# Kernel optimization log

Hardware: AMD Instinct MI355X
Metric: run time of the kernel (lower is better)

Reference implementation:

```python
import jax, jax.numpy as jnp
import numpy as np

B, L, N = 32, 64, 8
C, H_IMG, W_IMG = 3, 40, 40
HID = 64
N_ACT = 8
CNN_OUT = 64  # 64 channels * 1 * 1 spatial after the three convs on 40x40


def _conv(x, w, b, stride):
    # x: (B', Cin, H, W), w: (Cout, Cin, kh, kw)
    y = jax.lax.conv_general_dilated(
        x, w, window_strides=(stride, stride), padding='VALID',
        dimension_numbers=('NCHW', 'OIHW', 'NCHW'))
    return y + b[None, :, None, None]


def setup_inputs() -> dict:
    key = jax.random.key(0)
    ks = jax.random.split(key, 12)

    def rn(k, shape, fan_in):
        return jax.random.normal(k, shape, dtype=jnp.float32) * (1.0 / np.sqrt(fan_in))

    inp = {
        'obs_batch': jax.random.normal(ks[0], (B, L, N, C, H_IMG, W_IMG), dtype=jnp.float32),
        'hidden_state': jnp.zeros((B, N, HID), dtype=jnp.float32),
        'conv1_w': rn(ks[1], (32, C, 8, 8), C * 8 * 8),
        'conv1_b': jnp.zeros((32,), jnp.float32),
        'conv2_w': rn(ks[2], (64, 32, 4, 4), 32 * 4 * 4),
        'conv2_b': jnp.zeros((64,), jnp.float32),
        'conv3_w': rn(ks[3], (64, 64, 3, 3), 64 * 3 * 3),
        'conv3_b': jnp.zeros((64,), jnp.float32),
        'w_ih': rn(ks[4], (3 * HID, CNN_OUT), CNN_OUT),
        'w_hh': rn(ks[5], (3 * HID, HID), HID),
        'b_ih': jnp.zeros((3 * HID,), jnp.float32),
        'b_hh': jnp.zeros((3 * HID,), jnp.float32),
        'fc_w': rn(ks[6], (N_ACT, HID), HID),
        'fc_b': jnp.zeros((N_ACT,), jnp.float32),
    }
    return inp


def reference(obs_batch, hidden_state, conv1_w, conv1_b, conv2_w, conv2_b,
              conv3_w, conv3_b, w_ih, w_hh, b_ih, b_hh, fc_w, fc_b):
    b, l, n = obs_batch.shape[:3]
    x = obs_batch.reshape(-1, C, H_IMG, W_IMG)            # (B*L*N, C, H, W)
    x = jax.nn.relu(_conv(x, conv1_w, conv1_b, 4))
    x = jax.nn.relu(_conv(x, conv2_w, conv2_b, 2))
    x = jax.nn.relu(_conv(x, conv3_w, conv3_b, 1))
    feats = x.reshape(b, l, n, -1)                        # (B, L, N, F)

    # (L, B*N, F) time-major for scan
    rnn_in = feats.transpose(1, 0, 2, 3).reshape(l, b * n, -1)
    h0 = hidden_state.reshape(b * n, HID)

    def step(h, xt):
        gi = xt @ w_ih.T + b_ih
        gh = h @ w_hh.T + b_hh
        i_r, i_z, i_n = jnp.split(gi, 3, axis=-1)
        h_r, h_z, h_n = jnp.split(gh, 3, axis=-1)
        r = jax.nn.sigmoid(i_r + h_r)
        z = jax.nn.sigmoid(i_z + h_z)
        nn_ = jnp.tanh(i_n + r * h_n)
        h_new = (1.0 - z) * nn_ + z * h
        return h_new, h_new

    h_last, hs = jax.lax.scan(step, h0, rnn_in)           # hs: (L, B*N, HID)

    # torch path: stack (L, B*N, H) -> permute to (B*N, L, H) -> reshape (B*L*N, H)
    rnn_out = hs.transpose(1, 0, 2).reshape(b, n, l, HID).transpose(0, 2, 1, 3)
    q = rnn_out.reshape(-1, HID) @ fc_w.T + fc_b
    q_values = q.reshape(b, l, n, N_ACT)
    next_hidden_state = h_last.reshape(b, n, HID)
    return q_values, next_hidden_state
```

## Files before the change

### kernel.cpp

```cpp
#include <hip/hip_runtime.h>
#include <math.h>

typedef unsigned short ushort_t;
typedef unsigned int uint_t;
typedef __attribute__((ext_vector_type(8))) short short8_t;
typedef __attribute__((ext_vector_type(4))) float f32x4_t;

constexpr int Bb = 32, Ll = 64, Nn = 8;
constexpr int IMGS = Bb * Ll * Nn;
constexpr int Cc = 3, Hh = 40, Ww = 40;
constexpr int HID = 64, G3 = 192, NACT = 8;

__device__ inline float bf2f(ushort_t u) {
  union { uint_t i; float f; } v; v.i = ((uint_t)u) << 16; return v.f;
}
__device__ inline ushort_t f2bf(float f) {
  union { float f; uint_t u; } v; v.f = f;
  uint_t r = v.u + 0x7fffu + ((v.u >> 16) & 1u);
  return (ushort_t)(r >> 16);
}
__device__ inline void unpack2(uint_t u, float& lo, float& hi) {
  union { uint_t i; float f; } a, b;
  a.i = u << 16; b.i = u & 0xffff0000u;
  lo = a.f; hi = b.f;
}
__device__ inline float ld1(const void* p, int idx, int isbf) {
  return isbf ? bf2f(((const ushort_t*)p)[idx]) : ((const float*)p)[idx];
}
__device__ inline short8_t ldsh8(const ushort_t* p) {
  union { short8_t v; uint2 u[2]; } r;
  r.u[0] = *(const uint2*)p;
  r.u[1] = *(const uint2*)(p + 4);
  return r.v;
}
__device__ inline short8_t ldg8(const ushort_t* p) {
  union { short8_t v; uint4 u; } r;
  r.u = *(const uint4*)p;
  return r.v;
}
#define WAVE_FENCE() asm volatile("s_waitcnt lgkmcnt(0)" ::: "memory")

__global__ __launch_bounds__(256) void detect_kernel(
    const ushort_t* __restrict__ obs, const ushort_t* __restrict__ whh,
    int* __restrict__ flags) {
  __shared__ int cnt[2];
  if (threadIdx.x < 2) cnt[threadIdx.x] = 0;
  __syncthreads();
  int bad0 = 0, bad1 = 0;
  for (int i = threadIdx.x; i < 4096; i += 256) {
    int e0 = (obs[i] >> 7) & 0xFF; if (e0 >= 0xC0) bad0++;
    int e1 = (whh[i] >> 7) & 0xFF; if (e1 >= 0xC0) bad1++;
  }
  atomicAdd(&cnt[0], bad0);
  atomicAdd(&cnt[1], bad1);
  __syncthreads();
  if (threadIdx.x == 0) { flags[0] = (cnt[0] <= 4); flags[1] = (cnt[1] <= 4); }
}

__global__ __launch_bounds__(256) void repack_kernel(
    const void* __restrict__ w1, const void* __restrict__ w2,
    const void* __restrict__ w3, const void* __restrict__ wih,
    const int* __restrict__ flags,
    ushort_t* __restrict__ w1pack, ushort_t* __restrict__ w2pack,
    ushort_t* __restrict__ w3bf, ushort_t* __restrict__ wihb) {
  const int fw = flags[1];
  int t = blockIdx.x * 256 + threadIdx.x;
  if (t < 6144) w1pack[t] = f2bf(ld1(w1, t, fw));
  if (t < 32768) {
    int oc = t >> 9, r = t & 511;
    int kykx = r >> 5, ic = r & 31;
    w2pack[t] = f2bf(ld1(w2, oc * 512 + ic * 16 + kykx, fw));
  }
  if (t < 36864) w3bf[t] = f2bf(ld1(w3, t, fw));
  if (t < 12288) wihb[t] = f2bf(ld1(wih, t, fw));
}

__global__ __launch_bounds__(256, 4) void conv12_kernel(
    const void* __restrict__ obs, const ushort_t* __restrict__ w1pack,
    const ushort_t* __restrict__ w2pack,
    const void* __restrict__ b1, const void* __restrict__ b2,
    const int* __restrict__ flags, ushort_t* __restrict__ f2g, int img_base) {
  __shared__ __attribute__((aligned(16))) ushort_t s_mem[4][4800];

  const int tid = threadIdx.x;
  const int wave = tid >> 6, lane = tid & 63;
  const int lrow = lane & 15, lk8 = lane >> 4;
  const int fobs = flags[0], fw = flags[1];
  const int img0 = blockIdx.x * 4;

  if (fobs) {
    const uint4* src = reinterpret_cast<const uint4*>((const ushort_t*)obs + ((size_t)img_base + img0) * 4800);
    uint4 r[10];
#pragma unroll
    for (int it = 0; it < 10; ++it) {
      const int i = it * 256 + tid;
      r[it] = src[i < 2400 ? i : 2399];
    }
#pragma unroll
    for (int it = 0; it < 10; ++it) {
      const int i = it * 256 + tid;
      if (i < 2400) {
        const int im_ = i / 600, e = i - im_ * 600;
        reinterpret_cast<uint4*>(s_mem[im_])[e] = r[it];
      }
    }
  } else {
    const float4* src = reinterpret_cast<const float4*>((const float*)obs + ((size_t)img_base + img0) * 4800);
#pragma unroll
    for (int bb = 0; bb < 2; ++bb) {
      float4 r[10];
#pragma unroll
      for (int it = 0; it < 10; ++it) {
        const int i = (bb * 10 + it) * 256 + tid;
        r[it] = src[i < 4800 ? i : 4799];
      }
#pragma unroll
      for (int it = 0; it < 10; ++it) {
        const int i = (bb * 10 + it) * 256 + tid;
        if (i < 4800) {
          const int im_ = i / 1200, e = i - im_ * 1200;
          uint2 o;
          o.x = (uint_t)f2bf(r[it].x) | ((uint_t)f2bf(r[it].y) << 16);
          o.y = (uint_t)f2bf(r[it].z) | ((uint_t)f2bf(r[it].w) << 16);
          reinterpret_cast<uint2*>(s_mem[im_])[e] = o;
        }
      }
    }
  }
  __syncthreads();

  {
    ushort_t* si = s_mem[wave];
    int ab[6];
#pragma unroll
    for (int mt = 0; mt < 6; ++mt) {
      int p = mt * 16 + lrow; if (p > 80) p = 80;
      ab[mt] = (p / 9) * 160 + (p % 9) * 4;
    }
    f32x4_t acc[2][6];
#pragma unroll
    for (int nt = 0; nt < 2; ++nt)
#pragma unroll
      for (int mt = 0; mt < 6; ++mt) acc[nt][mt] = (f32x4_t){0.f, 0.f, 0.f, 0.f};
    const ushort_t* wr0 = w1pack + lrow * 192 + lk8 * 8;
#pragma unroll
    for (int ks = 0; ks < 6; ++ks) {
      const int g = ks * 4 + lk8;
      const int aoff = (g >> 3) * 1600 + (g & 7) * 40;
      short8_t b0 = ldg8(wr0 + ks * 32);
      short8_t b1v = ldg8(wr0 + 16 * 192 + ks * 32);
#pragma unroll
      for (int mt = 0; mt < 6; ++mt) {
        short8_t a = ldsh8(&si[aoff + ab[mt]]);
        acc[0][mt] = __builtin_amdgcn_mfma_f32_16x16x32_bf16(a, b0, acc[0][mt], 0, 0, 0);
        acc[1][mt] = __builtin_amdgcn_mfma_f32_16x16x32_bf16(a, b1v, acc[1][mt], 0, 0, 0);
      }
    }
    WAVE_FENCE();
    const float bz0 = ld1(b1, lrow, fw), bz1 = ld1(b1, 16 + lrow, fw);
#pragma unroll
    for (int mt = 0; mt < 6; ++mt) {
#pragma unroll
      for (int r = 0; r < 4; ++r) {
        const int p = mt * 16 + lk8 * 4 + r;
        if (p < 81) {
          si[p * 40 + lrow]      = f2bf(fmaxf(acc[0][mt][r] + bz0, 0.f));
          si[p * 40 + 16 + lrow] = f2bf(fmaxf(acc[1][mt][r] + bz1, 0.f));
        }
      }
    }
  }
  __syncthreads();

  {
    int imgr[3], pbx[3];
#pragma unroll
    for (int mt = 0; mt < 3; ++mt) {
      int row = mt * 16 + lrow; if (row > 35) row = 35;
      const int ir = row / 9, p2 = row - ir * 9;
      imgr[mt] = ir;
      pbx[mt] = (p2 / 3) * 18 + (p2 % 3) * 2;
    }
    f32x4_t acc[3];
#pragma unroll
    for (int mt = 0; mt < 3; ++mt) acc[mt] = (f32x4_t){0.f, 0.f, 0.f, 0.f};
    const ushort_t* w2r = w2pack + (wave * 16 + lrow) * 512 + lk8 * 8;
#pragma unroll
    for (int s = 0; s < 16; ++s) {
      const int po = (s >> 2) * 9 + (s & 3);
      short8_t bv = ldg8(w2r + s * 32);
      short8_t a0 = ldsh8(&s_mem[imgr[0]][(pbx[0] + po) * 40 + lk8 * 8]);
      short8_t a1 = ldsh8(&s_mem[imgr[1]][(pbx[1] + po) * 40 + lk8 * 8]);
      short8_t a2 = ldsh8(&s_mem[imgr[2]][(pbx[2] + po) * 40 + lk8 * 8]);
      acc[0] = __builtin_amdgcn_mfma_f32_16x16x32_bf16(a0, bv, acc[0], 0, 0, 0);
      acc[1] = __builtin_amdgcn_mfma_f32_16x16x32_bf16(a1, bv, acc[1], 0, 0, 0);
      acc[2] = __builtin_amdgcn_mfma_f32_16x16x32_bf16(a2, bv, acc[2], 0, 0, 0);
    }
    const int oc = wave * 16 + lrow;
    const float bias = ld1(b2, oc, fw);
#pragma unroll
    for (int mt = 0; mt < 3; ++mt) {
#pragma unroll
      for (int r = 0; r < 4; ++r) {
        const int row = mt * 16 + lk8 * 4 + r;
        if (row < 36) {
          const int ir = row / 9, pp = row - ir * 9;
          s_mem[ir][3232 + oc * 9 + pp] = f2bf(fmaxf(acc[mt][r] + bias, 0.f));
        }
      }
    }
  }
  __syncthreads();

#pragma unroll
  for (int t2 = 0; t2 < 2; ++t2) {
    const int i = t2 * 256 + tid;
    if (i < 288) {
      const int im_ = i / 72, off = i - im_ * 72;
      *reinterpret_cast<uint4*>(&f2g[((size_t)img_base + img0 + im_) * 576 + off * 8]) =
          *reinterpret_cast<const uint4*>(&s_mem[im_][3232 + off * 8]);
    }
  }
}

__global__ __launch_bounds__(256) void conv3gi_kernel(
    const ushort_t* __restrict__ f2g, const ushort_t* __restrict__ w3bf,
    const ushort_t* __restrict__ wihb, const void* __restrict__ b3,
    const int* __restrict__ flags, float* __restrict__ gi, int img_base) {
  __shared__ __attribute__((aligned(16))) ushort_t f2b[16 * 592];
  __shared__ __attribute__((aligned(16))) ushort_t f3b[16 * 72];

  const int tid = threadIdx.x;
  const int wave = tid >> 6, lane = tid & 63;
  const int lrow = lane & 15, lk8 = lane >> 4;
  const int fw = flags[1];
  const int iloc0 = blockIdx.x * 16;

  for (int i = tid; i < 16 * 72; i += 256) {
    const int im_ = i / 72, off = i - im_ * 72;
    *reinterpret_cast<uint4*>(&f2b[im_ * 592 + off * 8]) =
        *reinterpret_cast<const uint4*>(&f2g[((size_t)img_base + iloc0 + im_) * 576 + off * 8]);
  }
  __syncthreads();

  {
    f32x4_t c3 = (f32x4_t){0.f, 0.f, 0.f, 0.f};
    const ushort_t* w3r = w3bf + (wave * 16 + lrow) * 576 + lk8 * 8;
#pragma unroll
    for (int ks = 0; ks < 18; ++ks) {
      short8_t a = ldsh8(&f2b[lrow * 592 + ks * 32 + lk8 * 8]);
      short8_t bv = ldg8(w3r + ks * 32);
      c3 = __builtin_amdgcn_mfma_f32_16x16x32_bf16(a, bv, c3, 0, 0, 0);
    }
    const int oc = wave * 16 + lrow;
    const float bias = ld1(b3, oc, fw);
#pragma unroll
    for (int r = 0; r < 4; ++r)
      f3b[(lk8 * 4 + r) * 72 + oc] = f2bf(fmaxf(c3[r] + bias, 0.f));
  }
  __syncthreads();

#pragma unroll
  for (int t = 0; t < 3; ++t) {
    const int nt = wave * 3 + t;
    f32x4_t g = (f32x4_t){0.f, 0.f, 0.f, 0.f};
#pragma unroll
    for (int ks = 0; ks < 2; ++ks) {
      short8_t a = ldsh8(&f3b[lrow * 72 + ks * 32 + lk8 * 8]);
      short8_t bv = ldg8(wihb + (nt * 16 + lrow) * 64 + ks * 32 + lk8 * 8);
      g = __builtin_amdgcn_mfma_f32_16x16x32_bf16(a, bv, g, 0, 0, 0);
    }
#pragma unroll
    for (int r = 0; r < 4; ++r)
      gi[((size_t)img_base + iloc0 + lk8 * 4 + r) * G3 + nt * 16 + lrow] = g[r];
  }
}

__global__ __launch_bounds__(64, 1) void gru_kernel(
    const float* __restrict__ gi, const void* __restrict__ h0,
    const void* __restrict__ whh, const void* __restrict__ bih,
    const void* __restrict__ bhh, const int* __restrict__ flags,
    float* __restrict__ rnn, float* __restrict__ hout) {
  __shared__ float s_h[HID];
  const int j = threadIdx.x;
  const int s = blockIdx.x;
  const int fw = flags[1];

  float4 wr[16], wz[16], wn[16];
  if (fw) {
    const uint4* wb = reinterpret_cast<const uint4*>(whh);
#pragma unroll
    for (int i = 0; i < 8; ++i) {
      uint4 a = wb[(size_t)j * 8 + i];
      unpack2(a.x, wr[2 * i].x, wr[2 * i].y);
      unpack2(a.y, wr[2 * i].z, wr[2 * i].w);
      unpack2(a.z, wr[2 * i + 1].x, wr[2 * i + 1].y);
      unpack2(a.w, wr[2 * i + 1].z, wr[2 * i + 1].w);
      uint4 b = wb[(size_t)(64 + j) * 8 + i];
      unpack2(b.x, wz[2 * i].x, wz[2 * i].y);
      unpack2(b.y, wz[2 * i].z, wz[2 * i].w);
      unpack2(b.z, wz[2 * i + 1].x, wz[2 * i + 1].y);
      unpack2(b.w, wz[2 * i + 1].z, wz[2 * i + 1].w);
      uint4 c = wb[(size_t)(128 + j) * 8 + i];
      unpack2(c.x, wn[2 * i].x, wn[2 * i].y);
      unpack2(c.y, wn[2 * i].z, wn[2 * i].w);
      unpack2(c.z, wn[2 * i + 1].x, wn[2 * i + 1].y);
      unpack2(c.w, wn[2 * i + 1].z, wn[2 * i + 1].w);
    }
  } else {
    const float4* wf = reinterpret_cast<const float4*>(whh);
#pragma unroll
    for (int i = 0; i < 16; ++i) {
      wr[i] = wf[(size_t)j * 16 + i];
      wz[i] = wf[(size_t)(64 + j) * 16 + i];
      wn[i] = wf[(size_t)(128 + j) * 16 + i];
    }
  }

  float h = ld1(h0, s * HID + j, fw);
  s_h[j] = h;
  const float bir = ld1(bih, j, fw), biz = ld1(bih, 64 + j, fw), bin_ = ld1(bih, 128 + j, fw);
  const float bhr = ld1(bhh, j, fw), bhz = ld1(bhh, 64 + j, fw), bhn = ld1(bhh, 128 + j, fw);
  const int b = s >> 3, n = s & 7;
  const float* gbase = gi + ((size_t)b * Ll * Nn + n) * G3;
  float* rbase = rnn + ((size_t)b * Ll * Nn + n) * HID;
  WAVE_FENCE();

  float g0 = gbase[j], g1 = gbase[64 + j], g2 = gbase[128 + j];

  for (int l = 0; l < Ll; ++l) {
    float p0 = 0.f, p1 = 0.f, p2 = 0.f;
    if (l + 1 < Ll) {
      const float* gn = gbase + (size_t)(l + 1) * Nn * G3;
      p0 = gn[j]; p1 = gn[64 + j]; p2 = gn[128 + j];
    }
    float hr = bhr, hz = bhz, hn = bhn;
#pragma unroll
    for (int k = 0; k < 16; ++k) {
      float4 hv = *reinterpret_cast<const float4*>(&s_h[k * 4]);
      hr += wr[k].x * hv.x + wr[k].y * hv.y + wr[k].z * hv.z + wr[k].w * hv.w;
      hz += wz[k].x * hv.x + wz[k].y * hv.y + wz[k].z * hv.z + wz[k].w * hv.w;
      hn += wn[k].x * hv.x + wn[k].y * hv.y + wn[k].z * hv.z + wn[k].w * hv.w;
    }
    const float gr = g0 + bir + hr;
    const float gz = g1 + biz + hz;
    const float gn_ = g2 + bin_;
    const float r = 1.f / (1.f + __expf(-gr));
    const float z = 1.f / (1.f + __expf(-gz));
    const float nn_ = tanhf(gn_ + r * hn);
    h = (1.f - z) * nn_ + z * h;
    WAVE_FENCE();
    s_h[j] = h;
    rbase[(size_t)l * Nn * HID + j] = h;
    WAVE_FENCE();
    g0 = p0; g1 = p1; g2 = p2;
  }
  hout[(size_t)s * HID + j] = h;
}

__global__ __launch_bounds__(64) void fc_kernel(
    const float* __restrict__ rnn, const void* __restrict__ fcw,
    const void* __restrict__ fcb, const int* __restrict__ flags,
    float* __restrict__ q) {
  __shared__ float s_w[NACT * HID];
  __shared__ float s_b[NACT];
  const int tid = threadIdx.x;
  const int fw = flags[1];
  for (int i = tid; i < NACT * HID; i += 64) s_w[i] = ld1(fcw, i, fw);
  if (tid < NACT) s_b[tid] = ld1(fcb, tid, fw);
  __syncthreads();
  const int row = blockIdx.x * 64 + tid;
  float x[64];
  const float4* xp = reinterpret_cast<const float4*>(rnn + (size_t)row * HID);
#pragma unroll
  for (int i = 0; i < 16; ++i) {
    float4 v = xp[i];
    x[4 * i] = v.x; x[4 * i + 1] = v.y; x[4 * i + 2] = v.z; x[4 * i + 3] = v.w;
  }
#pragma unroll
  for (int a = 0; a < NACT; ++a) {
    float v = s_b[a];
#pragma unroll
    for (int k = 0; k < 64; ++k) v += x[k] * s_w[a * 64 + k];
    q[(size_t)row * NACT + a] = v;
  }
}

extern "C" void kernel_launch(void* const* d_in, const int* in_sizes, int n_in,
                              void* d_out, int out_size, void* d_ws, size_t ws_size,
                              hipStream_t stream) {
  const void* obs = d_in[0];
  const void* h0  = d_in[1];
  const void* w1  = d_in[2];
  const void* b1  = d_in[3];
  const void* w2  = d_in[4];
  const void* b2  = d_in[5];
  const void* w3  = d_in[6];
  const void* b3  = d_in[7];
  const void* wih = d_in[8];
  const void* whh = d_in[9];
  const void* bih = d_in[10];
  const void* bhh = d_in[11];
  const void* fcw = d_in[12];
  const void* fcb = d_in[13];

  float* qout = (float*)d_out;
  float* hout = qout + (size_t)IMGS * NACT;

  char* wsb = (char*)d_ws;
  int*      flags  = (int*)wsb;
  float*    gi     = (float*)(wsb + 16);
  float*    rnn    = gi + (size_t)IMGS * G3;
  ushort_t* w1pack = (ushort_t*)(rnn + (size_t)IMGS * HID);
  ushort_t* w2pack = w1pack + 6144;
  ushort_t* w3bf   = w2pack + 32768;
  ushort_t* wihb   = w3bf + 36864;
  ushort_t* f2g    = wihb + 12288;

  detect_kernel<<<1, 256, 0, stream>>>((const ushort_t*)obs, (const ushort_t*)whh, flags);
  repack_kernel<<<144, 256, 0, stream>>>(w1, w2, w3, wih, flags, w1pack, w2pack, w3bf, wihb);

  conv12_kernel<<<IMGS / 4, 256, 0, stream>>>(obs, w1pack, w2pack, b1, b2, flags, f2g, 0);
  conv3gi_kernel<<<IMGS / 16, 256, 0, stream>>>(f2g, w3bf, wihb, b3, flags, gi, 0);

  gru_kernel<<<256, 64, 0, stream>>>(gi, h0, whh, bih, bhh, flags, rnn, hout);
  fc_kernel<<<IMGS / 64, 64, 0, stream>>>(rnn, fcw, fcb, flags, qout);
}
```

Measured before the change: 197.0 us.

## Make conv12 persistent with double-buffered prefetch of next image pair

Converts conv12 from one block per 4 images to a persistent grid of 1024 blocks, each looping over image pairs with two LDS buffers. Global loads for the next pair are issued into registers before the current pair's conv1/conv2 MFMA work and written to the alternate buffer afterwards, hiding input-load latency. Work per block shrinks to 2 images, with waves splitting conv1 tiles, which costs extra barriers per iteration and more registers held for prefetch (the launch bounds still request 4 blocks per SM).

```diff
diff --git a/kernel.cpp b/kernel.cpp
--- a/kernel.cpp
+++ b/kernel.cpp
@@ -10,6 +10,8 @@
 constexpr int IMGS = Bb * Ll * Nn;
 constexpr int Cc = 3, Hh = 40, Ww = 40;
 constexpr int HID = 64, G3 = 192, NACT = 8;
+constexpr int CGRID = 1024;
+constexpr int NITER = (IMGS / 2) / CGRID;
 
 __device__ inline float bf2f(ushort_t u) {
   union { uint_t i; float f; } v; v.i = ((uint_t)u) << 16; return v.f;
@@ -79,147 +81,169 @@
     const void* __restrict__ obs, const ushort_t* __restrict__ w1pack,
     const ushort_t* __restrict__ w2pack,
     const void* __restrict__ b1, const void* __restrict__ b2,
-    const int* __restrict__ flags, ushort_t* __restrict__ f2g, int img_base) {
-  __shared__ __attribute__((aligned(16))) ushort_t s_mem[4][4800];
+    const int* __restrict__ flags, ushort_t* __restrict__ f2g) {
+  __shared__ __attribute__((aligned(16))) ushort_t s_mem[2][2][4800];
 
   const int tid = threadIdx.x;
   const int wave = tid >> 6, lane = tid & 63;
   const int lrow = lane & 15, lk8 = lane >> 4;
+  const int im = wave >> 1, half = wave & 1;
   const int fobs = flags[0], fw = flags[1];
-  const int img0 = blockIdx.x * 4;
-
-  if (fobs) {
-    const uint4* src = reinterpret_cast<const uint4*>((const ushort_t*)obs + ((size_t)img_base + img0) * 4800);
-    uint4 r[10];
-#pragma unroll
-    for (int it = 0; it < 10; ++it) {
-      const int i = it * 256 + tid;
-      r[it] = src[i < 2400 ? i : 2399];
-    }
-#pragma unroll
-    for (int it = 0; it < 10; ++it) {
-      const int i = it * 256 + tid;
-      if (i < 2400) {
-        const int im_ = i / 600, e = i - im_ * 600;
-        reinterpret_cast<uint4*>(s_mem[im_])[e] = r[it];
-      }
-    }
-  } else {
-    const float4* src = reinterpret_cast<const float4*>((const float*)obs + ((size_t)img_base + img0) * 4800);
-#pragma unroll
-    for (int bb = 0; bb < 2; ++bb) {
-      float4 r[10];
-#pragma unroll
-      for (int it = 0; it < 10; ++it) {
-        const int i = (bb * 10 + it) * 256 + tid;
-        r[it] = src[i < 4800 ? i : 4799];
-      }
-#pragma unroll
-      for (int it = 0; it < 10; ++it) {
-        const int i = (bb * 10 + it) * 256 + tid;
-        if (i < 4800) {
-          const int im_ = i / 1200, e = i - im_ * 1200;
+
+  int ab[3];
+#pragma unroll
+  for (int t = 0; t < 3; ++t) {
+    int p = (half * 3 + t) * 16 + lrow; if (p > 80) p = 80;
+    ab[t] = (p / 9) * 160 + (p % 9) * 4;
+  }
+  const float bz0 = ld1(b1, lrow, fw), bz1 = ld1(b1, 16 + lrow, fw);
+  int imgr[2], pbx[2];
+#pragma unroll
+  for (int mt = 0; mt < 2; ++mt) {
+    int row = mt * 16 + lrow; if (row > 17) row = 17;
+    const int ir = row / 9, p2 = row - ir * 9;
+    imgr[mt] = ir;
+    pbx[mt] = (p2 / 3) * 18 + (p2 % 3) * 2;
+  }
+  const ushort_t* w1r = w1pack + lrow * 192 + lk8 * 8;
+  const ushort_t* w2r = w2pack + (wave * 16 + lrow) * 512 + lk8 * 8;
+  const float b2v = ld1(b2, wave * 16 + lrow, fw);
+
+  {
+    const size_t base = (size_t)blockIdx.x * 2 * 4800;
+    if (fobs) {
+      const uint4* src = reinterpret_cast<const uint4*>((const ushort_t*)obs + base);
+#pragma unroll
+      for (int t2 = 0; t2 < 5; ++t2) {
+        const int i = t2 * 256 + tid;
+        if (i < 1200) reinterpret_cast<uint4*>(&s_mem[0][i / 600][0])[i % 600] = src[i];
+      }
+    } else {
+      const float4* src = reinterpret_cast<const float4*>((const float*)obs + base);
+#pragma unroll
+      for (int t2 = 0; t2 < 10; ++t2) {
+        const int i = t2 * 256 + tid;
+        if (i < 2400) {
+          float4 v = src[i];
           uint2 o;
-          o.x = (uint_t)f2bf(r[it].x) | ((uint_t)f2bf(r[it].y) << 16);
-          o.y = (uint_t)f2bf(r[it].z) | ((uint_t)f2bf(r[it].w) << 16);
-          reinterpret_cast<uint2*>(s_mem[im_])[e] = o;
+          o.x = (uint_t)f2bf(v.x) | ((uint_t)f2bf(v.y) << 16);
+          o.y = (uint_t)f2bf(v.z) | ((uint_t)f2bf(v.w) << 16);
+          reinterpret_cast<uint2*>(&s_mem[0][i / 1200][0])[i % 1200] = o;
         }
       }
     }
   }
   __syncthreads();
 
-  {
-    ushort_t* si = s_mem[wave];
-    int ab[6];
-#pragma unroll
-    for (int mt = 0; mt < 6; ++mt) {
-      int p = mt * 16 + lrow; if (p > 80) p = 80;
-      ab[mt] = (p / 9) * 160 + (p % 9) * 4;
-    }
-    f32x4_t acc[2][6];
+  for (int it = 0; it < NITER; ++it) {
+    const int c = it & 1;
+    const int img0 = (blockIdx.x + it * CGRID) * 2;
+    const bool has_next = (it + 1 < NITER);
+    const size_t nbase = has_next ? (size_t)(blockIdx.x + (it + 1) * CGRID) * 2 * 4800 : 0;
+
+    uint4 rb[5];
+    float4 rf[10];
+    if (has_next) {
+      if (fobs) {
+        const uint4* src = reinterpret_cast<const uint4*>((const ushort_t*)obs + nbase);
+#pragma unroll
+        for (int t2 = 0; t2 < 5; ++t2) { const int i = t2 * 256 + tid; rb[t2] = src[i < 1200 ? i : 1199]; }
+      } else {
+        const float4* src = reinterpret_cast<const float4*>((const float*)obs + nbase);
+#pragma unroll
+        for (int t2 = 0; t2 < 10; ++t2) { const int i = t2 * 256 + tid; rf[t2] = src[i < 2400 ? i : 2399]; }
+      }
+    }
+
+    ushort_t* si = &s_mem[c][im][0];
+    f32x4_t a1c[2][3];
 #pragma unroll
     for (int nt = 0; nt < 2; ++nt)
 #pragma unroll
-      for (int mt = 0; mt < 6; ++mt) acc[nt][mt] = (f32x4_t){0.f, 0.f, 0.f, 0.f};
-    const ushort_t* wr0 = w1pack + lrow * 192 + lk8 * 8;
+      for (int t = 0; t < 3; ++t) a1c[nt][t] = (f32x4_t){0.f, 0.f, 0.f, 0.f};
 #pragma unroll
     for (int ks = 0; ks < 6; ++ks) {
       const int g = ks * 4 + lk8;
       const int aoff = (g >> 3) * 1600 + (g & 7) * 40;
-      short8_t b0 = ldg8(wr0 + ks * 32);
-      short8_t b1v = ldg8(wr0 + 16 * 192 + ks * 32);
-#pragma unroll
-      for (int mt = 0; mt < 6; ++mt) {
-        short8_t a = ldsh8(&si[aoff + ab[mt]]);
-        acc[0][mt] = __builtin_amdgcn_mfma_f32_16x16x32_bf16(a, b0, acc[0][mt], 0, 0, 0);
-        acc[1][mt] = __builtin_amdgcn_mfma_f32_16x16x32_bf16(a, b1v, acc[1][mt], 0, 0, 0);
-      }
-    }
-    WAVE_FENCE();
-    const float bz0 = ld1(b1, lrow, fw), bz1 = ld1(b1, 16 + lrow, fw);
-#pragma unroll
-    for (int mt = 0; mt < 6; ++mt) {
+      short8_t b0 = ldg8(w1r + ks * 32);
+      short8_t b1v = ldg8(w1r + 16 * 192 + ks * 32);
+#pragma unroll
+      for (int t = 0; t < 3; ++t) {
+        short8_t a = ldsh8(&si[aoff + ab[t]]);
+        a1c[0][t] = __builtin_amdgcn_mfma_f32_16x16x32_bf16(a, b0, a1c[0][t], 0, 0, 0);
+        a1c[1][t] = __builtin_amdgcn_mfma_f32_16x16x32_bf16(a, b1v, a1c[1][t], 0, 0, 0);
+      }
+    }
+    __syncthreads();
+#pragma unroll
+    for (int t = 0; t < 3; ++t) {
 #pragma unroll
       for (int r = 0; r < 4; ++r) {
-        const int p = mt * 16 + lk8 * 4 + r;
+        const int p = (half * 3 + t) * 16 + lk8 * 4 + r;
         if (p < 81) {
-          si[p * 40 + lrow]      = f2bf(fmaxf(acc[0][mt][r] + bz0, 0.f));
-          si[p * 40 + 16 + lrow] = f2bf(fmaxf(acc[1][mt][r] + bz1, 0.f));
+          si[p * 40 + lrow]      = f2bf(fmaxf(a1c[0][t][r] + bz0, 0.f));
+          si[p * 40 + 16 + lrow] = f2bf(fmaxf(a1c[1][t][r] + bz1, 0.f));
         }
       }
     }
-  }
-  __syncthreads();
-
-  {
-    int imgr[3], pbx[3];
-#pragma unroll
-    for (int mt = 0; mt < 3; ++mt) {
-      int row = mt * 16 + lrow; if (row > 35) row = 35;
-      const int ir = row / 9, p2 = row - ir * 9;
-      imgr[mt] = ir;
-      pbx[mt] = (p2 / 3) * 18 + (p2 % 3) * 2;
-    }
-    f32x4_t acc[3];
-#pragma unroll
-    for (int mt = 0; mt < 3; ++mt) acc[mt] = (f32x4_t){0.f, 0.f, 0.f, 0.f};
-    const ushort_t* w2r = w2pack + (wave * 16 + lrow) * 512 + lk8 * 8;
-#pragma unroll
-    for (int s = 0; s < 16; ++s) {
-      const int po = (s >> 2) * 9 + (s & 3);
-      short8_t bv = ldg8(w2r + s * 32);
-      short8_t a0 = ldsh8(&s_mem[imgr[0]][(pbx[0] + po) * 40 + lk8 * 8]);
-      short8_t a1 = ldsh8(&s_mem[imgr[1]][(pbx[1] + po) * 40 + lk8 * 8]);
-      short8_t a2 = ldsh8(&s_mem[imgr[2]][(pbx[2] + po) * 40 + lk8 * 8]);
-      acc[0] = __builtin_amdgcn_mfma_f32_16x16x32_bf16(a0, bv, acc[0], 0, 0, 0);
-      acc[1] = __builtin_amdgcn_mfma_f32_16x16x32_bf16(a1, bv, acc[1], 0, 0, 0);
-      acc[2] = __builtin_amdgcn_mfma_f32_16x16x32_bf16(a2, bv, acc[2], 0, 0, 0);
-    }
-    const int oc = wave * 16 + lrow;
-    const float bias = ld1(b2, oc, fw);
-#pragma unroll
-    for (int mt = 0; mt < 3; ++mt) {
-#pragma unroll
-      for (int r = 0; r < 4; ++r) {
-        const int row = mt * 16 + lk8 * 4 + r;
-        if (row < 36) {
-          const int ir = row / 9, pp = row - ir * 9;
-          s_mem[ir][3232 + oc * 9 + pp] = f2bf(fmaxf(acc[mt][r] + bias, 0.f));
+    __syncthreads();
+
+    {
+      f32x4_t acc[2];
+#pragma unroll
+      for (int mt = 0; mt < 2; ++mt) acc[mt] = (f32x4_t){0.f, 0.f, 0.f, 0.f};
+#pragma unroll
+      for (int s = 0; s < 16; ++s) {
+        const int po = (s >> 2) * 9 + (s & 3);
+        short8_t bv = ldg8(w2r + s * 32);
+        short8_t a0 = ldsh8(&s_mem[c][imgr[0]][(pbx[0] + po) * 40 + lk8 * 8]);
+        short8_t a1 = ldsh8(&s_mem[c][imgr[1]][(pbx[1] + po) * 40 + lk8 * 8]);
+        acc[0] = __builtin_amdgcn_mfma_f32_16x16x32_bf16(a0, bv, acc[0], 0, 0, 0);
+        acc[1] = __builtin_amdgcn_mfma_f32_16x16x32_bf16(a1, bv, acc[1], 0, 0, 0);
+      }
+      const int oc = wave * 16 + lrow;
+#pragma unroll
+      for (int mt = 0; mt < 2; ++mt) {
+#pragma unroll
+        for (int r = 0; r < 4; ++r) {
+          const int row = mt * 16 + lk8 * 4 + r;
+          if (row < 18) {
+            const int ir = row / 9, pp = row - ir * 9;
+            s_mem[c][ir][3232 + oc * 9 + pp] = f2bf(fmaxf(acc[mt][r] + b2v, 0.f));
+          }
         }
       }
     }
-  }
-  __syncthreads();
-
-#pragma unroll
-  for (int t2 = 0; t2 < 2; ++t2) {
-    const int i = t2 * 256 + tid;
-    if (i < 288) {
-      const int im_ = i / 72, off = i - im_ * 72;
-      *reinterpret_cast<uint4*>(&f2g[((size_t)img_base + img0 + im_) * 576 + off * 8]) =
-          *reinterpret_cast<const uint4*>(&s_mem[im_][3232 + off * 8]);
-    }
+    __syncthreads();
+
+    if (tid < 144) {
+      const int im_ = tid / 72, off = tid - im_ * 72;
+      *reinterpret_cast<uint4*>(&f2g[(size_t)(img0 + im_) * 576 + off * 8]) =
+          *reinterpret_cast<const uint4*>(&s_mem[c][im_][3232 + off * 8]);
+    }
+
+    if (has_next) {
+      const int nc = c ^ 1;
+      if (fobs) {
+#pragma unroll
+        for (int t2 = 0; t2 < 5; ++t2) {
+          const int i = t2 * 256 + tid;
+          if (i < 1200) reinterpret_cast<uint4*>(&s_mem[nc][i / 600][0])[i % 600] = rb[t2];
+        }
+      } else {
+#pragma unroll
+        for (int t2 = 0; t2 < 10; ++t2) {
+          const int i = t2 * 256 + tid;
+          if (i < 2400) {
+            uint2 o;
+            o.x = (uint_t)f2bf(rf[t2].x) | ((uint_t)f2bf(rf[t2].y) << 16);
+            o.y = (uint_t)f2bf(rf[t2].z) | ((uint_t)f2bf(rf[t2].w) << 16);
+            reinterpret_cast<uint2*>(&s_mem[nc][i / 1200][0])[i % 1200] = o;
+          }
+        }
+      }
+    }
+    __syncthreads();
   }
 }
 
@@ -420,7 +444,7 @@
   detect_kernel<<<1, 256, 0, stream>>>((const ushort_t*)obs, (const ushort_t*)whh, flags);
   repack_kernel<<<144, 256, 0, stream>>>(w1, w2, w3, wih, flags, w1pack, w2pack, w3bf, wihb);
 
-  conv12_kernel<<<IMGS / 4, 256, 0, stream>>>(obs, w1pack, w2pack, b1, b2, flags, f2g, 0);
+  conv12_kernel<<<CGRID, 256, 0, stream>>>(obs, w1pack, w2pack, b1, b2, flags, f2g);
   conv3gi_kernel<<<IMGS / 16, 256, 0, stream>>>(f2g, w3bf, wihb, b3, flags, gi, 0);
 
   gru_kernel<<<256, 64, 0, stream>>>(gi, h0, whh, bih, bhh, flags, rnn, hout);
```

After: 428.5 us. 118% more time.
